# Performance work log

Hardware: AMD Instinct MI355X
Metric: run time of the kernel (lower is better)

## Reference

```python
import jax, jax.numpy as jnp
import numpy as np

B, T, H, W, D, NH = 8, 16, 14, 14, 768, 12
HID = int(D * 4.0)
HEAD_DIM = D // NH
EPS = 1e-5


def _ln(x, w, b):
    m = x.mean(-1, keepdims=True)
    v = ((x - m) ** 2).mean(-1, keepdims=True)
    return (x - m) * jax.lax.rsqrt(v + EPS) * w + b


def _attn(x, qkv_w, proj_w, proj_b):
    # x: [Bn, S, D]; qkv_w: [D, 3D] (no bias); proj: [D, D] + bias
    Bn, S, _ = x.shape
    qkv = (x @ qkv_w).reshape(Bn, S, 3, NH, HEAD_DIM).transpose(2, 0, 3, 1, 4)
    q, k, v = qkv[0], qkv[1], qkv[2]
    a = jnp.einsum('bhqd,bhkd->bhqk', q, k) * (HEAD_DIM ** -0.5)
    a = jax.nn.softmax(a, axis=-1)
    o = jnp.einsum('bhqk,bhkd->bhqd', a, v).transpose(0, 2, 1, 3).reshape(Bn, S, D)
    return o @ proj_w + proj_b


def setup_inputs() -> dict:
    key = jax.random.key(0)
    ks = jax.random.split(key, 20)
    N = H * W * T
    s = 0.02
    f32 = jnp.float32
    return {
        'x': jax.random.normal(ks[0], (B, 1 + N, D), f32),
        'tn1_w': jnp.ones((D,), f32), 'tn1_b': jnp.zeros((D,), f32),
        't_qkv_w': jax.random.normal(ks[1], (D, 3 * D), f32) * s,
        't_proj_w': jax.random.normal(ks[2], (D, D), f32) * s,
        't_proj_b': jnp.zeros((D,), f32),
        'tfc_w': jax.random.normal(ks[3], (D, D), f32) * s,
        'tfc_b': jnp.zeros((D,), f32),
        'n1_w': jnp.ones((D,), f32), 'n1_b': jnp.zeros((D,), f32),
        's_qkv_w': jax.random.normal(ks[4], (D, 3 * D), f32) * s,
        's_proj_w': jax.random.normal(ks[5], (D, D), f32) * s,
        's_proj_b': jnp.zeros((D,), f32),
        'n2_w': jnp.ones((D,), f32), 'n2_b': jnp.zeros((D,), f32),
        'fc1_w': jax.random.normal(ks[6], (D, HID), f32) * s,
        'fc1_b': jnp.zeros((HID,), f32),
        'fc2_w': jax.random.normal(ks[7], (HID, D), f32) * s,
        'fc2_b': jnp.zeros((D,), f32),
        'pt_mask': jnp.ones((B, 1 + N), dtype=bool),
        't_frames': T, 'height': H, 'width': W,
    }


def reference(x, tn1_w, tn1_b, t_qkv_w, t_proj_w, t_proj_b, tfc_w, tfc_b,
              n1_w, n1_b, s_qkv_w, s_proj_w, s_proj_b, n2_w, n2_b,
              fc1_w, fc1_b, fc2_w, fc2_b, pt_mask, t_frames, height, width):
    # divided space-time attention; USE_CLS_TOKEN=True, use_pt_visibility=False
    b = x.shape[0]
    t, h, w = t_frames, height, width
    n = h * w * t
    # --- temporal attention over t per (b, h, w) ---
    xt = x[:, 1:, :].reshape(b * h * w, t, D)  # 'b (h w t) m -> (b h w) t m'
    rt = _attn(_ln(xt, tn1_w, tn1_b), t_qkv_w, t_proj_w, t_proj_b)
    rt = rt.reshape(b, n, D) @ tfc_w + tfc_b  # temporal_fc
    xt2 = x[:, 1:, :] + rt
    init_cls = x[:, 0:1, :]  # [b, 1, D]
    # --- spatial attention over (1 + h*w) per (b, t) ---
    cls_tok = jnp.broadcast_to(init_cls, (b, t, D)).reshape(b * t, 1, D)
    xs = xt2.reshape(b, h * w, t, D).transpose(0, 2, 1, 3).reshape(b * t, h * w, D)
    xs = jnp.concatenate([cls_tok, xs], axis=1)  # [(b t), 1+hw, D]
    rs = _attn(_ln(xs, n1_w, n1_b), s_qkv_w, s_proj_w, s_proj_b)
    cls_out = rs[:, 0, :].reshape(b, t, D).mean(axis=1, keepdims=True)
    rs = rs[:, 1:, :].reshape(b, t, h * w, D).transpose(0, 2, 1, 3).reshape(b, n, D)
    x_new = jnp.concatenate([init_cls, xt2], axis=1) + jnp.concatenate([cls_out, rs], axis=1)
    # --- MLP block ---
    y = _ln(x_new, n2_w, n2_b)
    y = jax.nn.gelu(y @ fc1_w + fc1_b, approximate=False) @ fc2_w + fc2_b
    return x_new + y
```

## Files before the change

kernel.cpp:

```cpp
#include <hip/hip_runtime.h>
#include <cstdint>

using u16 = unsigned short;
using u32 = unsigned int;

typedef __bf16 bf16x8 __attribute__((ext_vector_type(8)));
typedef float  floatx4 __attribute__((ext_vector_type(4)));

#define DEV static __device__ __forceinline__

DEV u16 f2bf(float f) {
    u32 u = __float_as_uint(f);
    u += 0x7FFFu + ((u >> 16) & 1u);
    return (u16)(u >> 16);
}
DEV float bf2f(u16 v) { return __uint_as_float(((u32)v) << 16); }

DEV floatx4 mfma32(bf16x8 a, bf16x8 b, floatx4 c) {
    return __builtin_amdgcn_mfma_f32_16x16x32_bf16(a, b, c, 0, 0, 0);
}

DEV floatx4 fzero() { floatx4 z; z[0]=0.f; z[1]=0.f; z[2]=0.f; z[3]=0.f; return z; }

typedef __attribute__((address_space(3))) u32 as3_u32;
typedef __attribute__((address_space(1))) u32 as1_u32;

DEV void async_ld16(const u16* g, u16* l) {
    __builtin_amdgcn_global_load_lds(
        (const as1_u32*)g, (as3_u32*)l, 16, 0, 0);
}

__global__ __launch_bounds__(256) void transpose_w(
    const float* __restrict__ W, u16* __restrict__ Wt, int K, int N)
{
    __shared__ float t[32][33];
    const int tx = threadIdx.x, ty = threadIdx.y;
    const int gx = blockIdx.x * 32;
    const int gy = blockIdx.y * 32;
    #pragma unroll
    for (int i = 0; i < 4; ++i)
        t[ty + i*8][tx] = W[(size_t)(gy + ty + i*8) * N + gx + tx];
    __syncthreads();
    #pragma unroll
    for (int i = 0; i < 4; ++i)
        Wt[(size_t)(gx + ty + i*8) * K + gy + tx] = f2bf(t[tx][ty + i*8]);
}

template<int MODE>
__global__ __launch_bounds__(256) void ln_kernel(
    const float* __restrict__ xp, const u16* __restrict__ xt2,
    const float* __restrict__ w, const float* __restrict__ b,
    u16* __restrict__ out, int nrows)
{
    const int row = blockIdx.x * 4 + (threadIdx.x >> 6);
    if (row >= nrows) return;
    const int lane = threadIdx.x & 63;
    float vals[12];
    if constexpr (MODE == 0) {
        const float* src = xp + (size_t)(row + row/3136 + 1) * 768;
        #pragma unroll
        for (int j = 0; j < 3; ++j) {
            float4 v = reinterpret_cast<const float4*>(src)[j*64 + lane];
            vals[j*4+0]=v.x; vals[j*4+1]=v.y; vals[j*4+2]=v.z; vals[j*4+3]=v.w;
        }
    } else {
        const int bt = row / 197;
        const int p  = row - bt * 197;
        const int b0 = bt >> 4, tt = bt & 15;
        if (p == 0) {
            const float* src = xp + (size_t)b0 * 3137 * 768;
            #pragma unroll
            for (int j = 0; j < 3; ++j) {
                float4 v = reinterpret_cast<const float4*>(src)[j*64 + lane];
                vals[j*4+0]=v.x; vals[j*4+1]=v.y; vals[j*4+2]=v.z; vals[j*4+3]=v.w;
            }
        } else {
            const u16* src = xt2 + (size_t)(b0*3136 + (p-1)*16 + tt) * 768;
            #pragma unroll
            for (int j = 0; j < 3; ++j) {
                uint2 q = reinterpret_cast<const uint2*>(src)[j*64 + lane];
                vals[j*4+0] = bf2f((u16)(q.x & 0xFFFF));
                vals[j*4+1] = bf2f((u16)(q.x >> 16));
                vals[j*4+2] = bf2f((u16)(q.y & 0xFFFF));
                vals[j*4+3] = bf2f((u16)(q.y >> 16));
            }
        }
    }
    float s = 0.f, ss = 0.f;
    #pragma unroll
    for (int e = 0; e < 12; ++e) { s += vals[e]; ss += vals[e]*vals[e]; }
    #pragma unroll
    for (int o = 32; o > 0; o >>= 1) { s += __shfl_xor(s, o); ss += __shfl_xor(ss, o); }
    const float mean = s * (1.f/768.f);
    const float var  = ss * (1.f/768.f) - mean*mean;
    const float rstd = rsqrtf(var + 1e-5f);
    #pragma unroll
    for (int j = 0; j < 3; ++j) {
        const int c4 = (j*64 + lane) * 4;
        union { u16 u[4]; uint2 q; } o;
        #pragma unroll
        for (int e = 0; e < 4; ++e)
            o.u[e] = f2bf((vals[j*4+e] - mean)*rstd*w[c4+e] + b[c4+e]);
        *reinterpret_cast<uint2*>(&out[(size_t)row*768 + c4]) = o.q;
    }
}

__global__ __launch_bounds__(256) void combine_ln2(
    const float* __restrict__ xp, const u16* __restrict__ xt2,
    const u16* __restrict__ rsb, const float* __restrict__ w, const float* __restrict__ b,
    float* __restrict__ xnew, u16* __restrict__ ln2, int nrows)
{
    const int row = blockIdx.x * 4 + (threadIdx.x >> 6);
    if (row >= nrows) return;
    const int lane = threadIdx.x & 63;
    const int b0 = row / 3137;
    const int j  = row - b0 * 3137;
    float vals[12];
    if (j == 0) {
        #pragma unroll
        for (int e = 0; e < 12; ++e) {
            const int c = e*64 + lane;
            float acc = 0.f;
            for (int t = 0; t < 16; ++t)
                acc += bf2f(rsb[(size_t)(b0*16 + t) * 197 * 768 + c]);
            vals[e] = xp[(size_t)row*768 + c] + acc * (1.f/16.f);
        }
    } else {
        const int n_idx = j - 1;
        const int hw = n_idx >> 4, tt = n_idx & 15;
        const u16* a  = xt2 + (size_t)(b0*3136 + n_idx) * 768;
        const u16* r2 = rsb + (size_t)((b0*16 + tt)*197 + 1 + hw) * 768;
        #pragma unroll
        for (int e = 0; e < 12; ++e) {
            const int c = e*64 + lane;
            vals[e] = bf2f(a[c]) + bf2f(r2[c]);
        }
    }
    float s = 0.f, ss = 0.f;
    #pragma unroll
    for (int e = 0; e < 12; ++e) { s += vals[e]; ss += vals[e]*vals[e]; }
    #pragma unroll
    for (int o = 32; o > 0; o >>= 1) { s += __shfl_xor(s, o); ss += __shfl_xor(ss, o); }
    const float mean = s * (1.f/768.f);
    const float var  = ss * (1.f/768.f) - mean*mean;
    const float rstd = rsqrtf(var + 1e-5f);
    #pragma unroll
    for (int e = 0; e < 12; ++e) {
        const int c = e*64 + lane;
        xnew[(size_t)row*768 + c] = vals[e];
        ln2[(size_t)row*768 + c]  = f2bf((vals[e] - mean)*rstd*w[c] + b[c]);
    }
}

template<int RESID, bool BIAS, bool GELU_ACT, bool OUTF, bool OUTB, bool MASKM>
__global__ __launch_bounds__(256) void gemm_bt(
    const u16* __restrict__ A, const u16* __restrict__ Bt,
    const float* __restrict__ bias, const float* __restrict__ resid,
    float* __restrict__ Cf, u16* __restrict__ Cb,
    int N, int K, int lda, int ldb, int Mvalid)
{
    __shared__ __attribute__((aligned(16))) u16 smem[2*128*32];
    u16* As = smem;
    u16* Bs = smem + 128*32;
    const int tid  = threadIdx.x;
    const int wave = tid >> 6;
    const int lane = tid & 63;
    const int m15  = lane & 15;
    const int quad = lane >> 4;
    const int wm = wave >> 1, wn = wave & 1;
    const long m0 = (long)blockIdx.y * 128;
    const long n0 = (long)blockIdx.x * 128;

    const int s0 = wave*128 + lane;
    const int s1 = s0 + 64;
    const int kc0 = (s0 & 3) ^ ((s0 >> 3) & 3);
    const int kc1 = (s1 & 3) ^ ((s1 >> 3) & 3);
    const u16* Ag0 = A  + (size_t)(m0 + (s0 >> 2)) * lda + kc0 * 8;
    const u16* Ag1 = A  + (size_t)(m0 + (s1 >> 2)) * lda + kc1 * 8;
    const u16* Bg0 = Bt + (size_t)(n0 + (s0 >> 2)) * ldb + kc0 * 8;
    const u16* Bg1 = Bt + (size_t)(n0 + (s1 >> 2)) * ldb + kc1 * 8;
    u16* Al0 = &As[(wave*2 + 0) * 512];
    u16* Al1 = &As[(wave*2 + 1) * 512];
    u16* Bl0 = &Bs[(wave*2 + 0) * 512];
    u16* Bl1 = &Bs[(wave*2 + 1) * 512];

    const int swz = (quad ^ ((m15 >> 1) & 3)) * 8;

    floatx4 acc[4][4];
    #pragma unroll
    for (int i = 0; i < 4; ++i)
        #pragma unroll
        for (int j = 0; j < 4; ++j) acc[i][j] = fzero();

    for (int k0 = 0; k0 < K; k0 += 32) {
        __syncthreads();
        async_ld16(Ag0 + k0, Al0);
        async_ld16(Ag1 + k0, Al1);
        async_ld16(Bg0 + k0, Bl0);
        async_ld16(Bg1 + k0, Bl1);
        __syncthreads();
        bf16x8 af[4], bf[4];
        #pragma unroll
        for (int i = 0; i < 4; ++i)
            af[i] = *reinterpret_cast<const bf16x8*>(&As[(wm*64 + i*16 + m15)*32 + swz]);
        #pragma unroll
        for (int j = 0; j < 4; ++j)
            bf[j] = *reinterpret_cast<const bf16x8*>(&Bs[(wn*64 + j*16 + m15)*32 + swz]);
        #pragma unroll
        for (int i = 0; i < 4; ++i)
            #pragma unroll
            for (int j = 0; j < 4; ++j)
                acc[i][j] = mfma32(af[i], bf[j], acc[i][j]);
    }

    float bv[4];
    #pragma unroll
    for (int j = 0; j < 4; ++j)
        bv[j] = BIAS ? bias[n0 + wn*64 + j*16 + m15] : 0.f;

    if constexpr (OUTB) {
        u16* cbuf = smem + wave * 2048;
        #pragma unroll
        for (int p = 0; p < 2; ++p) {
            __syncthreads();
            #pragma unroll
            for (int ii = 0; ii < 2; ++ii) {
                const int i = p*2 + ii;
                #pragma unroll
                for (int j = 0; j < 4; ++j) {
                    #pragma unroll
                    for (int r = 0; r < 4; ++r) {
                        const long row = m0 + wm*64 + i*16 + quad*4 + r;
                        float v = acc[i][j][r] + bv[j];
                        if constexpr (RESID == 1)
                            v += resid[(size_t)row * N + (n0 + wn*64 + j*16 + m15)];
                        if constexpr (RESID == 2)
                            v += resid[(size_t)(row + row/3136 + 1) * 768 + (n0 + wn*64 + j*16 + m15)];
                        if constexpr (GELU_ACT)
                            v = 0.5f * v * (1.f + erff(v * 0.70710678118f));
                        cbuf[(ii*16 + quad*4 + r)*64 + j*16 + m15] = f2bf(v);
                    }
                }
            }
            __syncthreads();
            #pragma unroll
            for (int it = 0; it < 4; ++it) {
                const int lr = (lane >> 3) + it*8;
                const int cc = lane & 7;
                const uint4 val = *reinterpret_cast<const uint4*>(&cbuf[lr*64 + cc*8]);
                const long grow = m0 + wm*64 + p*32 + lr;
                *reinterpret_cast<uint4*>(&Cb[(size_t)grow * N + n0 + wn*64 + cc*8]) = val;
            }
        }
    } else {
        #pragma unroll
        for (int j = 0; j < 4; ++j) {
            const long col = n0 + wn*64 + j*16 + m15;
            #pragma unroll
            for (int i = 0; i < 4; ++i) {
                const long rowb = m0 + wm*64 + i*16 + quad*4;
                #pragma unroll
                for (int r = 0; r < 4; ++r) {
                    const long row = rowb + r;
                    if constexpr (MASKM) { if (row >= Mvalid) continue; }
                    float v = acc[i][j][r] + bv[j];
                    if constexpr (RESID == 1) v += resid[(size_t)row * N + col];
                    if constexpr (RESID == 2) v += resid[(size_t)(row + row/3136 + 1) * 768 + col];
                    if constexpr (GELU_ACT)   v = 0.5f * v * (1.f + erff(v * 0.70710678118f));
                    if constexpr (OUTF) Cf[(size_t)row * N + col] = v;
                }
            }
        }
    }
}

template<int S, int NQ, int NIT>
__global__ __launch_bounds__(256) void attn_kernel(
    const u16* __restrict__ qkv, u16* __restrict__ out, int ntask)
{
    __shared__ __attribute__((aligned(16))) u16 P_lds[4][16*32];
    const int wave = threadIdx.x >> 6;
    const int lane = threadIdx.x & 63;
    const int task = blockIdx.x * 4 + wave;
    if (task >= ntask) return;
    const int seq  = task / (12 * NQ);
    const int rem  = task - seq * (12 * NQ);
    const int head = rem / NQ;
    const int qt   = rem - head * NQ;
    const int m15  = lane & 15;
    const int quad = lane >> 4;
    const size_t base = (size_t)seq * S;

    const u16* qp = qkv + (base + qt*16 + m15) * 2304 + head*64 + quad*8;
    const bf16x8 Qf0 = *reinterpret_cast<const bf16x8*>(qp);
    const bf16x8 Qf1 = *reinterpret_cast<const bf16x8*>(qp + 32);

    floatx4 Oacc[4];
    #pragma unroll
    for (int c = 0; c < 4; ++c) Oacc[c] = fzero();
    float mrun = -__builtin_inff();
    float lrun = 0.f;
    u16* P = &P_lds[wave][0];

    for (int it = 0; it < NIT; ++it) {
        const int j0 = it * 32;
        floatx4 st[2];
        #pragma unroll
        for (int h2 = 0; h2 < 2; ++h2) {
            const u16* kp = qkv + (base + j0 + h2*16 + m15) * 2304 + 768 + head*64 + quad*8;
            const bf16x8 K0 = *reinterpret_cast<const bf16x8*>(kp);
            const bf16x8 K1 = *reinterpret_cast<const bf16x8*>(kp + 32);
            floatx4 z = fzero();
            z = mfma32(K0, Qf0, z);
            st[h2] = mfma32(K1, Qf1, z);
        }
        float sc[8];
        #pragma unroll
        for (int h2 = 0; h2 < 2; ++h2)
            #pragma unroll
            for (int r = 0; r < 4; ++r) {
                const int jj = j0 + h2*16 + quad*4 + r;
                sc[h2*4+r] = (jj < S) ? st[h2][r] * 0.125f : -__builtin_inff();
            }
        float tmax = sc[0];
        #pragma unroll
        for (int k = 1; k < 8; ++k) tmax = fmaxf(tmax, sc[k]);
        tmax = fmaxf(tmax, __shfl_xor(tmax, 16));
        tmax = fmaxf(tmax, __shfl_xor(tmax, 32));
        const float mnew = fmaxf(mrun, tmax);
        float p[8], tsum = 0.f;
        #pragma unroll
        for (int k = 0; k < 8; ++k) { p[k] = __expf(sc[k] - mnew); tsum += p[k]; }
        tsum += __shfl_xor(tsum, 16);
        tsum += __shfl_xor(tsum, 32);
        const float alpha = __expf(mrun - mnew);
        lrun = lrun * alpha + tsum;
        mrun = mnew;
        #pragma unroll
        for (int r = 0; r < 4; ++r) {
            const float ar = __shfl(alpha, quad*4 + r);
            #pragma unroll
            for (int c = 0; c < 4; ++c) Oacc[c][r] *= ar;
        }
        #pragma unroll
        for (int h2 = 0; h2 < 2; ++h2)
            #pragma unroll
            for (int r = 0; r < 4; ++r)
                P[m15*32 + h2*16 + quad*4 + r] = f2bf(p[h2*4+r]);
        const bf16x8 Pf = *reinterpret_cast<const bf16x8*>(&P[m15*32 + quad*8]);
        #pragma unroll
        for (int c = 0; c < 4; ++c) {
            union { u16 u[8]; bf16x8 v; } vf;
            #pragma unroll
            for (int jj2 = 0; jj2 < 8; ++jj2)
                vf.u[jj2] = qkv[(base + j0 + quad*8 + jj2) * 2304 + 1536 + head*64 + c*16 + m15];
            Oacc[c] = mfma32(Pf, vf.v, Oacc[c]);
        }
    }
    const float linv_self = 1.f / lrun;
    #pragma unroll
    for (int r = 0; r < 4; ++r) {
        const int prow = qt*16 + quad*4 + r;
        const float linv = __shfl(linv_self, quad*4 + r);
        if (prow < S) {
            u16* op = out + (base + prow) * 768 + head*64 + m15;
            #pragma unroll
            for (int c = 0; c < 4; ++c) op[c*16] = f2bf(Oacc[c][r] * linv);
        }
    }
}

extern "C" void kernel_launch(void* const* d_in, const int* in_sizes, int n_in,
                              void* d_out, int out_size, void* d_ws, size_t ws_size,
                              hipStream_t stream)
{
    (void)in_sizes; (void)n_in; (void)out_size; (void)ws_size;
    const float* x        = (const float*)d_in[0];
    const float* tn1_w    = (const float*)d_in[1];
    const float* tn1_b    = (const float*)d_in[2];
    const float* t_qkv_w  = (const float*)d_in[3];
    const float* t_proj_w = (const float*)d_in[4];
    const float* t_proj_b = (const float*)d_in[5];
    const float* tfc_w    = (const float*)d_in[6];
    const float* tfc_b    = (const float*)d_in[7];
    const float* n1_w     = (const float*)d_in[8];
    const float* n1_b     = (const float*)d_in[9];
    const float* s_qkv_w  = (const float*)d_in[10];
    const float* s_proj_w = (const float*)d_in[11];
    const float* s_proj_b = (const float*)d_in[12];
    const float* n2_w     = (const float*)d_in[13];
    const float* n2_b     = (const float*)d_in[14];
    const float* fc1_w    = (const float*)d_in[15];
    const float* fc1_b    = (const float*)d_in[16];
    const float* fc2_w    = (const float*)d_in[17];
    const float* fc2_b    = (const float*)d_in[18];
    float* out = (float*)d_out;

    char* ws = (char*)d_ws;
    size_t off = 0;
    auto alloc = [&](size_t bytes) -> void* {
        void* p = ws + off;
        off += (bytes + 255) & ~(size_t)255;
        return p;
    };
    u16* wt_tqkv  = (u16*)alloc((size_t)768*2304*2);
    u16* wt_tproj = (u16*)alloc((size_t)768*768*2);
    u16* wt_tfc   = (u16*)alloc((size_t)768*768*2);
    u16* wt_sqkv  = (u16*)alloc((size_t)768*2304*2);
    u16* wt_sproj = (u16*)alloc((size_t)768*768*2);
    u16* wt_fc1   = (u16*)alloc((size_t)768*3072*2);
    u16* wt_fc2   = (u16*)alloc((size_t)3072*768*2);
    u16* slotA = (u16*)alloc((size_t)25280*2304*2);
    u16* slotB = (u16*)alloc((size_t)25216*768*2);
    u16* slotD = (u16*)alloc((size_t)25216*768*2);
    u16* slotE = (u16*)alloc((size_t)25216*768*2);

    dim3 tb(32, 8);
    transpose_w<<<dim3(72, 24), tb, 0, stream>>>(t_qkv_w,  wt_tqkv,  768, 2304);
    transpose_w<<<dim3(24, 24), tb, 0, stream>>>(t_proj_w, wt_tproj, 768, 768);
    transpose_w<<<dim3(24, 24), tb, 0, stream>>>(tfc_w,    wt_tfc,   768, 768);
    transpose_w<<<dim3(72, 24), tb, 0, stream>>>(s_qkv_w,  wt_sqkv,  768, 2304);
    transpose_w<<<dim3(24, 24), tb, 0, stream>>>(s_proj_w, wt_sproj, 768, 768);
    transpose_w<<<dim3(96, 24), tb, 0, stream>>>(fc1_w,    wt_fc1,   768, 3072);
    transpose_w<<<dim3(24, 96), tb, 0, stream>>>(fc2_w,    wt_fc2,   3072, 768);

    u16* lnT  = slotD;
    u16* qkvT = slotA;
    ln_kernel<0><<<25088/4, 256, 0, stream>>>(x, nullptr, tn1_w, tn1_b, lnT, 25088);
    gemm_bt<0,false,false,false,true,false><<<dim3(18,196), 256, 0, stream>>>(
        lnT, wt_tqkv, nullptr, nullptr, nullptr, qkvT, 2304, 768, 768, 768, 0);

    u16* attnT = slotD;
    attn_kernel<16,1,1><<<18816/4, 256, 0, stream>>>(qkvT, attnT, 18816);

    u16* hp = slotE;
    gemm_bt<0,true,false,false,true,false><<<dim3(6,196), 256, 0, stream>>>(
        attnT, wt_tproj, t_proj_b, nullptr, nullptr, hp, 768, 768, 768, 768, 0);

    u16* xt2 = slotB;
    gemm_bt<2,true,false,false,true,false><<<dim3(6,196), 256, 0, stream>>>(
        hp, wt_tfc, tfc_b, x, nullptr, xt2, 768, 768, 768, 768, 0);

    u16* lnS = slotD;
    ln_kernel<1><<<25216/4, 256, 0, stream>>>(x, xt2, n1_w, n1_b, lnS, 25216);

    u16* qkvS = slotA;
    gemm_bt<0,false,false,false,true,false><<<dim3(18,197), 256, 0, stream>>>(
        lnS, wt_sqkv, nullptr, nullptr, nullptr, qkvS, 2304, 768, 768, 768, 0);

    u16* attnS = slotD;
    attn_kernel<197,13,7><<<19968/4, 256, 0, stream>>>(qkvS, attnS, 19968);

    u16* rsb = slotE;
    gemm_bt<0,true,false,false,true,false><<<dim3(6,197), 256, 0, stream>>>(
        attnS, wt_sproj, s_proj_b, nullptr, nullptr, rsb, 768, 768, 768, 768, 0);

    float* xnew = out;
    u16* ln2 = slotD;
    combine_ln2<<<25096/4, 256, 0, stream>>>(x, xt2, rsb, n2_w, n2_b, xnew, ln2, 25096);

    u16* h1 = slotA;
    for (int half = 0; half < 2; ++half) {
        const u16* w1h = wt_fc1 + (size_t)half * 1536 * 768;
        const float* b1h = fc1_b + half * 1536;
        gemm_bt<0,true,true,false,true,false><<<dim3(12,197), 256, 0, stream>>>(
            ln2, w1h, b1h, nullptr, nullptr, h1, 1536, 768, 768, 768, 0);
        const u16* w2h = wt_fc2 + (size_t)half * 1536;
        if (half == 0)
            gemm_bt<1,true,false,true,false,true><<<dim3(6,197), 256, 0, stream>>>(
                h1, w2h, fc2_b, out, out, nullptr, 768, 1536, 1536, 3072, 25096);
        else
            gemm_bt<1,false,false,true,false,true><<<dim3(6,197), 256, 0, stream>>>(
                h1, w2h, nullptr, out, out, nullptr, 768, 1536, 1536, 3072, 25096);
    }
}
```

Before: 1.417 ms.

## Fold temporal proj into temporal_fc, double-buffer GEMM LDS, remap workgroups across XCDs

```diff
diff --git a/kernel.cpp b/kernel.cpp
--- a/kernel.cpp
+++ b/kernel.cpp
@@ -44,6 +44,35 @@
     #pragma unroll
     for (int i = 0; i < 4; ++i)
         Wt[(size_t)(gx + ty + i*8) * K + gy + tx] = f2bf(t[tx][ty + i*8]);
+}
+
+__global__ __launch_bounds__(256) void cast_bf16(
+    const float* __restrict__ W, u16* __restrict__ o, int n4)
+{
+    const int i = blockIdx.x * 256 + threadIdx.x;
+    if (i < n4) {
+        float4 v = reinterpret_cast<const float4*>(W)[i];
+        union { u16 u[4]; uint2 q; } r;
+        r.u[0]=f2bf(v.x); r.u[1]=f2bf(v.y); r.u[2]=f2bf(v.z); r.u[3]=f2bf(v.w);
+        reinterpret_cast<uint2*>(o)[i] = r.q;
+    }
+}
+
+__global__ __launch_bounds__(256) void fuse_bias(
+    const float* __restrict__ pb, const float* __restrict__ Wf,
+    const float* __restrict__ bf, float* __restrict__ bc)
+{
+    const int n = blockIdx.x * 4 + (threadIdx.x >> 6);
+    const int lane = threadIdx.x & 63;
+    float s = 0.f;
+    #pragma unroll
+    for (int it = 0; it < 12; ++it) {
+        const int j = it*64 + lane;
+        s += pb[j] * Wf[(size_t)j * 768 + n];
+    }
+    #pragma unroll
+    for (int o = 32; o > 0; o >>= 1) s += __shfl_xor(s, o);
+    if (lane == 0) bc[n] = s + bf[n];
 }
 
 template<int MODE>
@@ -159,17 +188,26 @@
     float* __restrict__ Cf, u16* __restrict__ Cb,
     int N, int K, int lda, int ldb, int Mvalid)
 {
-    __shared__ __attribute__((aligned(16))) u16 smem[2*128*32];
-    u16* As = smem;
-    u16* Bs = smem + 128*32;
+    __shared__ __attribute__((aligned(16))) u16 smem[4*128*32];
     const int tid  = threadIdx.x;
     const int wave = tid >> 6;
     const int lane = tid & 63;
     const int m15  = lane & 15;
     const int quad = lane >> 4;
     const int wm = wave >> 1, wn = wave & 1;
-    const long m0 = (long)blockIdx.y * 128;
-    const long n0 = (long)blockIdx.x * 128;
+
+    const int gx = (int)gridDim.x;
+    const int nwg = gx * (int)gridDim.y;
+    int lid = (int)blockIdx.y * gx + (int)blockIdx.x;
+    {
+        const int q = nwg >> 3, r = nwg & 7;
+        const int c = lid & 7, idx = lid >> 3;
+        lid = (c < r ? c*(q+1) : r*(q+1) + (c-r)*q) + idx;
+    }
+    const int bx = lid % gx;
+    const int by = lid / gx;
+    const long m0 = (long)by * 128;
+    const long n0 = (long)bx * 128;
 
     const int s0 = wave*128 + lane;
     const int s1 = s0 + 64;
@@ -179,10 +217,6 @@
     const u16* Ag1 = A  + (size_t)(m0 + (s1 >> 2)) * lda + kc1 * 8;
     const u16* Bg0 = Bt + (size_t)(n0 + (s0 >> 2)) * ldb + kc0 * 8;
     const u16* Bg1 = Bt + (size_t)(n0 + (s1 >> 2)) * ldb + kc1 * 8;
-    u16* Al0 = &As[(wave*2 + 0) * 512];
-    u16* Al1 = &As[(wave*2 + 1) * 512];
-    u16* Bl0 = &Bs[(wave*2 + 0) * 512];
-    u16* Bl1 = &Bs[(wave*2 + 1) * 512];
 
     const int swz = (quad ^ ((m15 >> 1) & 3)) * 8;
 
@@ -192,25 +226,39 @@
         #pragma unroll
         for (int j = 0; j < 4; ++j) acc[i][j] = fzero();
 
-    for (int k0 = 0; k0 < K; k0 += 32) {
+    auto stg = [&](int k0, int dn) {
+        u16* base = smem + dn*8192;
+        async_ld16(Ag0 + k0, base + (wave*2+0)*512);
+        async_ld16(Ag1 + k0, base + (wave*2+1)*512);
+        async_ld16(Bg0 + k0, base + 4096 + (wave*2+0)*512);
+        async_ld16(Bg1 + k0, base + 4096 + (wave*2+1)*512);
+    };
+    auto comp = [&](int dn) {
+        const u16* base = smem + dn*8192;
+        bf16x8 af[4], bfr[4];
+        #pragma unroll
+        for (int i = 0; i < 4; ++i)
+            af[i] = *reinterpret_cast<const bf16x8*>(&base[(wm*64 + i*16 + m15)*32 + swz]);
+        #pragma unroll
+        for (int j = 0; j < 4; ++j)
+            bfr[j] = *reinterpret_cast<const bf16x8*>(&base[4096 + (wn*64 + j*16 + m15)*32 + swz]);
+        #pragma unroll
+        for (int i = 0; i < 4; ++i)
+            #pragma unroll
+            for (int j = 0; j < 4; ++j)
+                acc[i][j] = mfma32(af[i], bfr[j], acc[i][j]);
+    };
+
+    const int NK = K >> 5;
+    stg(0, 0);
+    __syncthreads();
+    for (int k = 0; k < NK; k += 2) {
+        stg((k+1) << 5, 1);
+        comp(0);
         __syncthreads();
-        async_ld16(Ag0 + k0, Al0);
-        async_ld16(Ag1 + k0, Al1);
-        async_ld16(Bg0 + k0, Bl0);
-        async_ld16(Bg1 + k0, Bl1);
+        if (k + 2 < NK) stg((k+2) << 5, 0);
+        comp(1);
         __syncthreads();
-        bf16x8 af[4], bf[4];
-        #pragma unroll
-        for (int i = 0; i < 4; ++i)
-            af[i] = *reinterpret_cast<const bf16x8*>(&As[(wm*64 + i*16 + m15)*32 + swz]);
-        #pragma unroll
-        for (int j = 0; j < 4; ++j)
-            bf[j] = *reinterpret_cast<const bf16x8*>(&Bs[(wn*64 + j*16 + m15)*32 + swz]);
-        #pragma unroll
-        for (int i = 0; i < 4; ++i)
-            #pragma unroll
-            for (int j = 0; j < 4; ++j)
-                acc[i][j] = mfma32(af[i], bf[j], acc[i][j]);
     }
 
     float bv[4];
@@ -404,8 +452,10 @@
         return p;
     };
     u16* wt_tqkv  = (u16*)alloc((size_t)768*2304*2);
-    u16* wt_tproj = (u16*)alloc((size_t)768*768*2);
+    u16* tproj_rm = (u16*)alloc((size_t)768*768*2);
     u16* wt_tfc   = (u16*)alloc((size_t)768*768*2);
+    u16* wt_comb  = (u16*)alloc((size_t)768*768*2);
+    float* bcomb  = (float*)alloc((size_t)768*4);
     u16* wt_sqkv  = (u16*)alloc((size_t)768*2304*2);
     u16* wt_sproj = (u16*)alloc((size_t)768*768*2);
     u16* wt_fc1   = (u16*)alloc((size_t)768*3072*2);
@@ -417,12 +467,16 @@
 
     dim3 tb(32, 8);
     transpose_w<<<dim3(72, 24), tb, 0, stream>>>(t_qkv_w,  wt_tqkv,  768, 2304);
-    transpose_w<<<dim3(24, 24), tb, 0, stream>>>(t_proj_w, wt_tproj, 768, 768);
     transpose_w<<<dim3(24, 24), tb, 0, stream>>>(tfc_w,    wt_tfc,   768, 768);
     transpose_w<<<dim3(72, 24), tb, 0, stream>>>(s_qkv_w,  wt_sqkv,  768, 2304);
     transpose_w<<<dim3(24, 24), tb, 0, stream>>>(s_proj_w, wt_sproj, 768, 768);
     transpose_w<<<dim3(96, 24), tb, 0, stream>>>(fc1_w,    wt_fc1,   768, 3072);
     transpose_w<<<dim3(24, 96), tb, 0, stream>>>(fc2_w,    wt_fc2,   3072, 768);
+    cast_bf16<<<576, 256, 0, stream>>>(t_proj_w, tproj_rm, 768*768/4);
+
+    gemm_bt<0,false,false,false,true,false><<<dim3(6,6), 256, 0, stream>>>(
+        wt_tfc, tproj_rm, nullptr, nullptr, nullptr, wt_comb, 768, 768, 768, 768, 0);
+    fuse_bias<<<192, 256, 0, stream>>>(t_proj_b, tfc_w, tfc_b, bcomb);
 
     u16* lnT  = slotD;
     u16* qkvT = slotA;
@@ -433,13 +487,9 @@
     u16* attnT = slotD;
     attn_kernel<16,1,1><<<18816/4, 256, 0, stream>>>(qkvT, attnT, 18816);
 
-    u16* hp = slotE;
-    gemm_bt<0,true,false,false,true,false><<<dim3(6,196), 256, 0, stream>>>(
-        attnT, wt_tproj, t_proj_b, nullptr, nullptr, hp, 768, 768, 768, 768, 0);
-
     u16* xt2 = slotB;
     gemm_bt<2,true,false,false,true,false><<<dim3(6,196), 256, 0, stream>>>(
-        hp, wt_tfc, tfc_b, x, nullptr, xt2, 768, 768, 768, 768, 0);
+        attnT, wt_comb, bcomb, x, nullptr, xt2, 768, 768, 768, 768, 0);
 
     u16* lnS = slotD;
     ln_kernel<1><<<25216/4, 256, 0, stream>>>(x, xt2, n1_w, n1_b, lnS, 25216);
```

After: 1.302 ms. 1.09x faster.
